# Optimization experiments

Measured on AMD Instinct MI355X. Metric: run time of the kernel, lower is better.

Reference implementation:

```python
import jax, jax.numpy as jnp
import numpy as np

N, IN_FEATS, H_FEATS, N_LAYERS, TOP_K, M = 8192, 512, 256, 2, 16, 65536


def setup_inputs() -> dict:
    key = jax.random.key(0)
    ks = jax.random.split(key, 16)
    s = 0.05
    return {
        "src": jax.random.randint(ks[0], (M,), 0, N, dtype=jnp.int32),
        "dst": jax.random.randint(ks[1], (M,), 0, N, dtype=jnp.int32),
        "labels": jax.random.uniform(ks[2], (M,), dtype=jnp.float32),
        "adj": jax.random.uniform(ks[3], (N, N), dtype=jnp.float32),
        "x": jax.random.normal(ks[4], (N, IN_FEATS), dtype=jnp.float32),
        # GNN1 layer weights
        "W1_0": jax.random.normal(ks[5], (IN_FEATS, H_FEATS), dtype=jnp.float32) * s,
        "W1_1": jax.random.normal(ks[6], (H_FEATS, H_FEATS), dtype=jnp.float32) * s,
        # GNN2 layer weights
        "W2_0": jax.random.normal(ks[7], (IN_FEATS, H_FEATS), dtype=jnp.float32) * s,
        "W2_1": jax.random.normal(ks[8], (H_FEATS, H_FEATS), dtype=jnp.float32) * s,
        # similarity-graph attention params
        "W": jax.random.normal(ks[9], (IN_FEATS, H_FEATS), dtype=jnp.float32) * s,
        "a1": jax.random.normal(ks[10], (H_FEATS, 1), dtype=jnp.float32) * s,
        "a2": jax.random.normal(ks[11], (H_FEATS, 1), dtype=jnp.float32) * s,
        # bilinear head: weight [1, in_feats, 2*h_feats], bias [1]
        "bil_w": jax.random.normal(ks[12], (1, IN_FEATS, 2 * H_FEATS), dtype=jnp.float32) * s,
        "bil_b": jnp.zeros((1,), dtype=jnp.float32),
    }


def _adj_norm(a):
    n = a.shape[0]
    a = a + jnp.eye(n, dtype=a.dtype)
    deg = a.sum(axis=0)[:, None]  # column sums, shape [n,1] (matches torch sum(dim=0).unsqueeze(1))
    return a / deg


def _gcn(a, x, weights):
    an = _adj_norm(a)
    z = x
    for Wl in weights:  # dropout=0.0 -> identity
        z = jax.nn.elu(an @ (z @ Wl))
    return z


def _sim_graph(x, W, a1, a2, top_k):
    n = x.shape[0]
    h = x @ W                      # [n, h]
    s1 = h @ a1                    # [n, 1]
    s2 = (h @ a2).reshape(1, n)    # [1, n]
    a = s1 + s2 - jnp.eye(n, dtype=x.dtype) * 1e15
    a = jax.nn.softmax(jax.nn.leaky_relu(a, 0.2), axis=1)
    kth = jax.lax.top_k(a, top_k)[0][:, -1:]  # k-th largest per row
    m = a >= kth
    m = m | m.T
    return m.astype(x.dtype)


def reference(src, dst, labels, adj, x, W1_0, W1_1, W2_0, W2_1, W, a1, a2, bil_w, bil_b):
    h = _gcn(adj, x, [W1_0, W1_1])
    sim_adj = _sim_graph(x, W, a1, a2, TOP_K)
    h_ = _gcn(sim_adj, x, [W2_0, W2_1])
    h_cat = jnp.concatenate([h, h_], axis=1)          # [n, 2h]
    src_h = x[src]                                    # [m, in_feats]
    dst_h = h_cat[dst]                                # [m, 2h]
    logits = jnp.einsum('mi,ij,mj->m', src_h, bil_w[0], dst_h) + bil_b[0]
    # BCEWithLogitsLoss (mean), numerically stable
    loss = jnp.mean(jnp.maximum(logits, 0.0) - logits * labels + jnp.log1p(jnp.exp(-jnp.abs(logits))))
    predict = logits >= 0
    return (loss, logits, predict)
```

## Files before the change

### kernel.cpp

```cpp
#include <hip/hip_runtime.h>
#include <math.h>

#define NN    8192
#define FIN   512
#define HF    256
#define ME    65536

typedef _Float16 f16x8 __attribute__((ext_vector_type(8)));
typedef __fp16 pk16x2 __attribute__((ext_vector_type(2)));
typedef float f32x4  __attribute__((ext_vector_type(4)));

__device__ inline void split_pk(float a0, float a1, unsigned& hi, unsigned& lo) {
    pk16x2 h = __builtin_amdgcn_cvt_pkrtz(a0, a1);
    float r0 = a0 - (float)h[0];
    float r1 = a1 - (float)h[1];
    pk16x2 l = __builtin_amdgcn_cvt_pkrtz(r0, r1);
    hi = __builtin_bit_cast(unsigned, h);
    lo = __builtin_bit_cast(unsigned, l);
}
__device__ inline unsigned pack_f16rn(float a0, float a1) {
    _Float16 h0 = (_Float16)a0, h1 = (_Float16)a1;
    unsigned u0 = (unsigned)__builtin_bit_cast(unsigned short, h0);
    unsigned u1 = (unsigned)__builtin_bit_cast(unsigned short, h1);
    return u0 | (u1 << 16);
}
__device__ inline void split_f16(float v, short& hi, short& lo) {
    _Float16 h = (_Float16)v;
    _Float16 l = (_Float16)(v - (float)h);
    hi = __builtin_bit_cast(short, h);
    lo = __builtin_bit_cast(short, l);
}
__device__ inline float eluf(float v) { return v > 0.f ? v : expm1f(v); }

__device__ inline void gload16(const void* g, void* l) {
    __builtin_amdgcn_global_load_lds(
        (const __attribute__((address_space(1))) unsigned int*)g,
        (__attribute__((address_space(3))) unsigned int*)l, 16, 0, 0);
}

__global__ __launch_bounds__(256) void colsum_deg(const float* __restrict__ adj,
                                                  float* __restrict__ deg) {
    int c = blockIdx.x * 256 + threadIdx.x;
    int r0 = blockIdx.y * 256;
    float s = 0.f;
    for (int r = r0; r < r0 + 256; ++r) s += adj[(size_t)r * NN + c];
    if (blockIdx.y == 0) s += 1.f;
    atomicAdd(&deg[c], s);
}

__global__ __launch_bounds__(256) void trans_w_split(const float* __restrict__ src,
                                                     short* __restrict__ dsth,
                                                     short* __restrict__ dstl,
                                                     int K, int lgN) {
    int idx = blockIdx.x * 256 + threadIdx.x;
    int N = 1 << lgN;
    int k = idx >> lgN, n = idx & (N - 1);
    short h, l;
    split_f16(src[idx], h, l);
    dsth[(size_t)n * K + k] = h;
    dstl[(size_t)n * K + k] = l;
}

__global__ __launch_bounds__(256, 2) void mfma_split(
    const float* __restrict__ A, const short* __restrict__ BtH,
    const short* __restrict__ BtL, float* __restrict__ C,
    short* __restrict__ CtH, short* __restrict__ CtL, int M, int K, int N)
{
    __shared__ __align__(16) char smem[40960];
    char* sA  = smem;
    char* sBh = smem + 8192;
    char* sBl = smem + 24576;
    float* sT = (float*)smem;
    const int tid = threadIdx.x, lane = tid & 63, wid = tid >> 6;
    const int wm = wid >> 1, wn = wid & 1;
    const int m0 = blockIdx.x * 64, n0 = blockIdx.y * 128;
    const int lhi = lane >> 4, llo = lane & 15;

    f32x4 acc[2][4];
    #pragma unroll
    for (int mi = 0; mi < 2; ++mi)
        #pragma unroll
        for (int ni = 0; ni < 4; ++ni) acc[mi][ni] = (f32x4){0.f, 0.f, 0.f, 0.f};

    for (int kt = 0; kt < K; kt += 64) {
        float4 av[4];
        #pragma unroll
        for (int it = 0; it < 4; ++it) {
            int h = tid + 256 * it;
            int r = h >> 4, hs = h & 15, slot = hs >> 1, half = hs & 1;
            int gk = ((slot ^ (r & 7)) * 2 + half) * 4;
            av[it] = *(const float4*)(A + (size_t)(m0 + r) * K + kt + gk);
        }
        __syncthreads();
        #pragma unroll
        for (int it = 0; it < 4; ++it) {
            int u = tid + 256 * it;
            int c = u >> 3, s = u & 7;
            size_t off = (size_t)(n0 + c) * K + kt + (s ^ (c & 7)) * 8;
            gload16(BtH + off, sBh + u * 16);
            gload16(BtL + off, sBl + u * 16);
        }
        #pragma unroll
        for (int it = 0; it < 4; ++it) {
            int h = tid + 256 * it;
            uint2 wh;
            wh.x = pack_f16rn(av[it].x, av[it].y);
            wh.y = pack_f16rn(av[it].z, av[it].w);
            *(uint2*)(sA + h * 8) = wh;
        }
        __syncthreads();
        #pragma unroll
        for (int ks = 0; ks < 2; ++ks) {
            f16x8 af[2], bfh[4], bfl[4];
            #pragma unroll
            for (int mi = 0; mi < 2; ++mi) {
                int R = wm * 32 + mi * 16 + llo;
                int boff = R * 128 + (((ks * 4 + lhi) ^ (R & 7)) << 4);
                af[mi] = *(const f16x8*)(sA + boff);
            }
            #pragma unroll
            for (int ni = 0; ni < 4; ++ni) {
                int Cc = wn * 64 + ni * 16 + llo;
                int boff = Cc * 128 + (((ks * 4 + lhi) ^ (Cc & 7)) << 4);
                bfh[ni] = *(const f16x8*)(sBh + boff);
                bfl[ni] = *(const f16x8*)(sBl + boff);
            }
            #pragma unroll
            for (int mi = 0; mi < 2; ++mi)
                #pragma unroll
                for (int ni = 0; ni < 4; ++ni) {
                    acc[mi][ni] = __builtin_amdgcn_mfma_f32_16x16x32_f16(af[mi], bfh[ni], acc[mi][ni], 0, 0, 0);
                    acc[mi][ni] = __builtin_amdgcn_mfma_f32_16x16x32_f16(af[mi], bfl[ni], acc[mi][ni], 0, 0, 0);
                }
        }
    }

    __syncthreads();
    #pragma unroll
    for (int mi = 0; mi < 2; ++mi)
        #pragma unroll
        for (int ni = 0; ni < 4; ++ni) {
            int lr = wm * 32 + mi * 16 + lhi * 4;
            int lc = wn * 64 + ni * 16 + llo;
            int R0 = m0 + lr;
            int Cc = n0 + lc;
            #pragma unroll
            for (int r = 0; r < 4; ++r) {
                C[(size_t)(R0 + r) * N + Cc] = acc[mi][ni][r];
                sT[(lr + r) * 136 + lc] = acc[mi][ni][r];
            }
        }
    __syncthreads();
    int c = tid >> 1, ih = (tid & 1) * 32;
    unsigned bh[16], bl[16];
    #pragma unroll
    for (int j = 0; j < 32; j += 2)
        split_pk(sT[(ih + j) * 136 + c], sT[(ih + j + 1) * 136 + c],
                 bh[j >> 1], bl[j >> 1]);
    int4* dh = (int4*)(CtH + (size_t)(n0 + c) * M + m0 + ih);
    int4* dl = (int4*)(CtL + (size_t)(n0 + c) * M + m0 + ih);
    #pragma unroll
    for (int q = 0; q < 4; ++q) { dh[q] = ((int4*)bh)[q]; dl[q] = ((int4*)bl)[q]; }
}

__global__ __launch_bounds__(256, 4) void adj_prop(const float* __restrict__ adj,
                                                   const short* __restrict__ YtH,
                                                   const short* __restrict__ YtL,
                                                   float* part0, float* part1)
{
    __shared__ __align__(16) char smem[24576];
    const int tid = threadIdx.x, lane = tid & 63, wid = tid >> 6;
    const int wm = wid >> 1, wn = wid & 1;
    const int bid = blockIdx.x;
    const int g  = bid & 7;
    const int ky = g >> 2;
    const int gx = g & 3;
    const int s  = bid >> 3;
    const int bm = gx * 32 + (s >> 2), bn = s & 3;
    const int i0 = bm * 64, c0 = bn * 64;
    const int kbase = ky * (NN / 2);
    const int lhi = lane >> 4, llo = lane & 15;

    f32x4 acc[2][2];
    #pragma unroll
    for (int mi = 0; mi < 2; ++mi)
        #pragma unroll
        for (int ni = 0; ni < 2; ++ni) acc[mi][ni] = (f32x4){0.f, 0.f, 0.f, 0.f};

    float4 avA[4], avB[4];

#define LOAD_ADJ(KT, AV)                                                        \
    {                                                                           \
        _Pragma("unroll")                                                       \
        for (int it = 0; it < 4; ++it) {                                        \
            int h = tid + 256 * it;                                             \
            int r = h >> 4, hs = h & 15, slot = hs >> 1, half = hs & 1;         \
            int gk = ((slot ^ (r & 7)) * 2 + half) * 4;                         \
            AV[it] = *(const float4*)(adj + (size_t)(i0 + r) * NN + (KT) + gk); \
        }                                                                       \
    }

#define GLOAD_B(KT)                                                             \
    {                                                                           \
        char* bh = smem + 8192;                                                 \
        char* bl = smem + 16384;                                                \
        _Pragma("unroll")                                                       \
        for (int it = 0; it < 2; ++it) {                                        \
            int u = tid + 256 * it;                                             \
            int c = u >> 3, s2 = u & 7;                                         \
            size_t off = (size_t)(c0 + c) * NN + (KT) + (s2 ^ (c & 7)) * 8;     \
            gload16(YtH + off, bh + u * 16);                                    \
            gload16(YtL + off, bl + u * 16);                                    \
        }                                                                       \
    }

#define CONVERT_A(AV)                                                           \
    {                                                                           \
        char* ah = smem;                                                        \
        _Pragma("unroll")                                                       \
        for (int it = 0; it < 4; ++it) {                                        \
            int h = tid + 256 * it;                                             \
            uint2 wh;                                                           \
            wh.x = pack_f16rn(AV[it].x, AV[it].y);                              \
            wh.y = pack_f16rn(AV[it].z, AV[it].w);                              \
            *(uint2*)(ah + h * 8) = wh;                                         \
        }                                                                       \
    }

#define DO_MFMA()                                                               \
    {                                                                           \
        const char* ah = smem;                                                  \
        const char* bh = smem + 8192;                                           \
        const char* bl = smem + 16384;                                          \
        _Pragma("unroll")                                                       \
        for (int ks = 0; ks < 2; ++ks) {                                        \
            f16x8 af[2], bfh[2], bfl[2];                                        \
            _Pragma("unroll")                                                   \
            for (int mi = 0; mi < 2; ++mi) {                                    \
                int R = wm * 32 + mi * 16 + llo;                                \
                int boff = R * 128 + (((ks * 4 + lhi) ^ (R & 7)) << 4);         \
                af[mi] = *(const f16x8*)(ah + boff);                            \
            }                                                                   \
            _Pragma("unroll")                                                   \
            for (int ni = 0; ni < 2; ++ni) {                                    \
                int Cc = wn * 32 + ni * 16 + llo;                               \
                int boff = Cc * 128 + (((ks * 4 + lhi) ^ (Cc & 7)) << 4);       \
                bfh[ni] = *(const f16x8*)(bh + boff);                           \
                bfl[ni] = *(const f16x8*)(bl + boff);                           \
            }                                                                   \
            _Pragma("unroll")                                                   \
            for (int mi = 0; mi < 2; ++mi)                                      \
                _Pragma("unroll")                                               \
                for (int ni = 0; ni < 2; ++ni) {                                \
                    acc[mi][ni] = __builtin_amdgcn_mfma_f32_16x16x32_f16(af[mi], bfh[ni], acc[mi][ni], 0, 0, 0); \
                    acc[mi][ni] = __builtin_amdgcn_mfma_f32_16x16x32_f16(af[mi], bfl[ni], acc[mi][ni], 0, 0, 0); \
                }                                                               \
        }                                                                       \
    }

    LOAD_ADJ(kbase, avA);
    LOAD_ADJ(kbase + 64, avB);
    for (int t = 0; t < 64; t += 2) {
        __syncthreads();
        GLOAD_B(kbase + t * 64);
        CONVERT_A(avA);
        __syncthreads();
        if (t + 2 < 64) LOAD_ADJ(kbase + (t + 2) * 64, avA);
        DO_MFMA();
        __syncthreads();
        GLOAD_B(kbase + (t + 1) * 64);
        CONVERT_A(avB);
        __syncthreads();
        if (t + 3 < 64) LOAD_ADJ(kbase + (t + 3) * 64, avB);
        DO_MFMA();
    }
#undef LOAD_ADJ
#undef GLOAD_B
#undef CONVERT_A
#undef DO_MFMA

    __syncthreads();
    float* sT = (float*)smem;
    #pragma unroll
    for (int mi = 0; mi < 2; ++mi)
        #pragma unroll
        for (int ni = 0; ni < 2; ++ni) {
            int lr = wm * 32 + mi * 16 + lhi * 4;
            int lc = wn * 32 + ni * 16 + llo;
            #pragma unroll
            for (int r = 0; r < 4; ++r)
                sT[(lr + r) * 68 + lc] = acc[mi][ni][r];
        }
    __syncthreads();
    float* po = ky == 0 ? part0 : part1;
    int row = tid >> 2, quad = tid & 3;
    float4* prow = (float4*)(po + (size_t)(i0 + row) * HF + c0 + quad * 16);
    #pragma unroll
    for (int q = 0; q < 4; ++q)
        prow[q] = *(const float4*)&sT[row * 68 + quad * 16 + q * 4];
}

__global__ __launch_bounds__(256) void adj_reduce(const float* part0,
                                                  const float* part1,
                                                  const float* __restrict__ Y,
                                                  const float* __restrict__ deg,
                                                  float* H) {
    int idx = blockIdx.x * 256 + threadIdx.x;
    int i = idx >> 6;
    float4 p0 = ((const float4*)part0)[idx];
    float4 p1 = ((const float4*)part1)[idx];
    float4 y  = ((const float4*)Y)[idx];
    float dinv = 1.f / deg[i];
    float4 v;
    v.x = eluf((p0.x + p1.x + y.x) * dinv);
    v.y = eluf((p0.y + p1.y + y.y) * dinv);
    v.z = eluf((p0.z + p1.z + y.z) * dinv);
    v.w = eluf((p0.w + p1.w + y.w) * dinv);
    ((float4*)H)[idx] = v;
}

__global__ __launch_bounds__(256) void gemm32(
    const float* __restrict__ A, const float* __restrict__ B,
    float* __restrict__ C, int M, int K, int N)
{
    __shared__ __align__(16) float sA[32][68];
    __shared__ __align__(16) float sB[32][68];
    const int tid = threadIdx.x;
    const int r0 = blockIdx.x * 64, c0 = blockIdx.y * 64;
    const int tr = tid >> 4, tc = tid & 15;
    float acc[4][4];
    #pragma unroll
    for (int i = 0; i < 4; ++i)
        #pragma unroll
        for (int j = 0; j < 4; ++j) acc[i][j] = 0.f;

    for (int k0 = 0; k0 < K; k0 += 32) {
        float4 av[2], bv[2];
        #pragma unroll
        for (int it = 0; it < 2; ++it) {
            int u = tid + it * 256;
            int rr = u >> 3, kk = (u & 7) * 4;
            av[it] = *(const float4*)(A + (size_t)(r0 + rr) * K + k0 + kk);
        }
        #pragma unroll
        for (int it = 0; it < 2; ++it) {
            int u = tid + it * 256;
            int br = u >> 4, bc = (u & 15) * 4;
            bv[it] = *(const float4*)(B + (size_t)(k0 + br) * N + c0 + bc);
        }
        __syncthreads();
        #pragma unroll
        for (int it = 0; it < 2; ++it) {
            int u = tid + it * 256;
            int rr = u >> 3, kk = (u & 7) * 4;
            sA[kk + 0][rr] = av[it].x; sA[kk + 1][rr] = av[it].y;
            sA[kk + 2][rr] = av[it].z; sA[kk + 3][rr] = av[it].w;
        }
        #pragma unroll
        for (int it = 0; it < 2; ++it) {
            int u = tid + it * 256;
            int br = u >> 4, bc = (u & 15) * 4;
            *(float4*)&sB[br][bc] = bv[it];
        }
        __syncthreads();
        #pragma unroll
        for (int kk = 0; kk < 32; ++kk) {
            float4 a = *(const float4*)&sA[kk][4 * tr];
            float4 b = *(const float4*)&sB[kk][4 * tc];
            float aa[4] = {a.x, a.y, a.z, a.w};
            float bb[4] = {b.x, b.y, b.z, b.w};
            #pragma unroll
            for (int i = 0; i < 4; ++i)
                #pragma unroll
                for (int j = 0; j < 4; ++j)
                    acc[i][j] = fmaf(aa[i], bb[j], acc[i][j]);
        }
        __syncthreads();
    }
    #pragma unroll
    for (int i = 0; i < 4; ++i) {
        size_t off = (size_t)(r0 + 4 * tr + i) * N + c0 + 4 * tc;
        *(float4*)(C + off) = make_float4(acc[i][0], acc[i][1], acc[i][2], acc[i][3]);
    }
}

__global__ __launch_bounds__(512) void wa2_kernel(const float* __restrict__ W,
                                                  const float* __restrict__ a2,
                                                  float* __restrict__ wa2) {
    int i = threadIdx.x;
    float s = 0.f;
    for (int j = 0; j < HF; ++j) s += W[(size_t)i * HF + j] * a2[j];
    wa2[i] = s;
}

__global__ __launch_bounds__(256) void s2_kernel(const float* __restrict__ x,
                                                 const float* __restrict__ wa2,
                                                 float* __restrict__ s2) {
    int lane = threadIdx.x & 63, wv = threadIdx.x >> 6;
    int row = blockIdx.x * 4 + wv;
    const float4* xr = (const float4*)(x + (size_t)row * FIN);
    const float4* w4 = (const float4*)wa2;
    float s = 0.f;
    #pragma unroll
    for (int t = 0; t < 2; ++t) {
        float4 a = xr[lane + 64 * t], b = w4[lane + 64 * t];
        s += a.x * b.x + a.y * b.y + a.z * b.z + a.w * b.w;
    }
    #pragma unroll
    for (int off = 32; off > 0; off >>= 1) s += __shfl_down(s, off);
    if (lane == 0) s2[row] = s;
}

__global__ __launch_bounds__(256) void top16_kernel(const float* __restrict__ s2,
                                                    int* __restrict__ Tflag) {
    __shared__ float sv[NN];
    __shared__ float rv[256];
    __shared__ int   ri[256];
    int tid = threadIdx.x;
    for (int i = tid; i < NN; i += 256) sv[i] = s2[i];
    __syncthreads();
    for (int it = 0; it < 16; ++it) {
        float best = -INFINITY; int bi = NN;
        for (int i = tid; i < NN; i += 256) {
            float v = sv[i];
            if (v > best) { best = v; bi = i; }
        }
        rv[tid] = best; ri[tid] = bi;
        __syncthreads();
        for (int off = 128; off > 0; off >>= 1) {
            if (tid < off) {
                float v2 = rv[tid + off]; int i2 = ri[tid + off];
                if (v2 > rv[tid] || (v2 == rv[tid] && i2 < ri[tid])) {
                    rv[tid] = v2; ri[tid] = i2;
                }
            }
            __syncthreads();
        }
        if (tid == 0) { int wi = ri[0]; Tflag[wi] = 1; sv[wi] = -INFINITY; }
        __syncthreads();
    }
}

__global__ __launch_bounds__(256) void colsum_T(const float* __restrict__ Y,
                                                const int* __restrict__ Tflag,
                                                float* __restrict__ total,
                                                float* __restrict__ sumT) {
    int k = threadIdx.x;
    int r0 = blockIdx.x * 128;
    float t = 0.f, tt = 0.f;
    for (int r = r0; r < r0 + 128; ++r) {
        float v = Y[(size_t)r * HF + k];
        t += v;
        if (Tflag[r]) tt += v;
    }
    atomicAdd(&total[k], t);
    atomicAdd(&sumT[k], tt);
}

__global__ __launch_bounds__(256) void gcn2_combine(float* __restrict__ Y,
                                                    const int* __restrict__ Tflag,
                                                    const float* __restrict__ sumT,
                                                    const float* __restrict__ total) {
    int idx = blockIdx.x * 256 + threadIdx.x;
    int i = idx >> 8, k = idx & 255;
    float v;
    if (Tflag[i]) v = total[k] / 8192.0f;
    else          v = (sumT[k] + Y[idx]) / 17.0f;
    Y[idx] = v > 0.f ? v : expm1f(v);
}

__global__ __launch_bounds__(256) void bilinear_kernel(
    const float* __restrict__ XB, const float* __restrict__ H,
    const float* __restrict__ Hs, const int* __restrict__ src,
    const int* __restrict__ dst, const float* __restrict__ labels,
    const float* __restrict__ bil_b,
    float* __restrict__ out_logits, float* __restrict__ out_pred,
    float* __restrict__ partials)
{
    __shared__ float wterm[4];
    int lane = threadIdx.x & 63;
    int wv = threadIdx.x >> 6;
    int e = blockIdx.x * 4 + wv;
    int s = src[e], d = dst[e];
    const float4* xb = (const float4*)(XB + (size_t)s * 512);
    const float4* h1 = (const float4*)(H + (size_t)d * HF);
    const float4* h2 = (const float4*)(Hs + (size_t)d * HF);
    float4 a = xb[lane], b = h1[lane];
    float sum = a.x * b.x + a.y * b.y + a.z * b.z + a.w * b.w;
    a = xb[64 + lane]; b = h2[lane];
    sum += a.x * b.x + a.y * b.y + a.z * b.z + a.w * b.w;
    #pragma unroll
    for (int off = 32; off > 0; off >>= 1) sum += __shfl_down(sum, off);
    if (lane == 0) {
        float l = sum + bil_b[0];
        out_logits[e] = l;
        out_pred[e] = (l >= 0.f) ? 1.f : 0.f;
        float lab = labels[e];
        wterm[wv] = fmaxf(l, 0.f) - l * lab + log1pf(expf(-fabsf(l)));
    }
    __syncthreads();
    if (threadIdx.x == 0)
        partials[blockIdx.x] = wterm[0] + wterm[1] + wterm[2] + wterm[3];
}

__global__ __launch_bounds__(256) void loss_finalize(const float* __restrict__ partials,
                                                     float* __restrict__ out) {
    __shared__ float s[256];
    int tid = threadIdx.x;
    float t = 0.f;
    for (int i = tid; i < ME / 4; i += 256) t += partials[i];
    s[tid] = t; __syncthreads();
    for (int off = 128; off > 0; off >>= 1) {
        if (tid < off) s[tid] += s[tid + off];
        __syncthreads();
    }
    if (tid == 0) out[0] = s[0] * (1.0f / (float)ME);
}

extern "C" void kernel_launch(void* const* d_in, const int* in_sizes, int n_in,
                              void* d_out, int out_size, void* d_ws, size_t ws_size,
                              hipStream_t stream) {
    const int*   src    = (const int*)d_in[0];
    const int*   dst    = (const int*)d_in[1];
    const float* labels = (const float*)d_in[2];
    const float* adj    = (const float*)d_in[3];
    const float* x      = (const float*)d_in[4];
    const float* W1_0   = (const float*)d_in[5];
    const float* W1_1   = (const float*)d_in[6];
    const float* W2_0   = (const float*)d_in[7];
    const float* W2_1   = (const float*)d_in[8];
    const float* W      = (const float*)d_in[9];
    const float* a2     = (const float*)d_in[11];
    const float* bilw   = (const float*)d_in[12];
    const float* bilb   = (const float*)d_in[13];

    float* w = (float*)d_ws;
    float* deg    = w + 0;
    float* s2v    = w + 8192;
    float* wa2v   = w + 16384;
    float* sumT   = w + 16896;
    float* total  = w + 17152;
    float* sum2T  = w + 17408;
    float* tot2   = w + 17664;
    float* lossp  = w + 17920;
    int*   Tflag  = (int*)(w + 34304);
    short* W10tH  = (short*)(w + 42496);
    short* W10tL  = (short*)(w + 108032);
    short* W11tH  = (short*)(w + 173568);
    short* W11tL  = (short*)(w + 206336);
    float* bufY   = w + 239104;
    short* YbtH   = (short*)(w + 2336256);
    short* YbtL   = (short*)(w + 3384832);
    float* bufH1  = w + 4433408;
    float* bufH   = w + 6530560;
    float* bufHs  = w + 8627712;
    float* XB     = bufY;

    float* out       = (float*)d_out;
    float* out_logit = out + 1;
    float* out_pred  = out + 1 + ME;

    hipMemsetAsync(deg, 0, NN * sizeof(float), stream);
    hipMemsetAsync(sumT, 0, 1024 * sizeof(float), stream);
    hipMemsetAsync(Tflag, 0, NN * sizeof(int), stream);

    trans_w_split<<<512, 256, 0, stream>>>(W1_0, W10tH, W10tL, 512, 8);
    trans_w_split<<<256, 256, 0, stream>>>(W1_1, W11tH, W11tL, 256, 8);

    colsum_deg<<<dim3(32, 32), 256, 0, stream>>>(adj, deg);

    mfma_split<<<dim3(128, 2), 256, 0, stream>>>(x, W10tH, W10tL, bufY, YbtH, YbtL, NN, FIN, HF);
    adj_prop<<<1024, 256, 0, stream>>>(adj, YbtH, YbtL, bufH, bufHs);
    adj_reduce<<<2048, 256, 0, stream>>>(bufH, bufHs, bufY, deg, bufH1);
    mfma_split<<<dim3(128, 2), 256, 0, stream>>>(bufH1, W11tH, W11tL, bufY, YbtH, YbtL, NN, HF, HF);
    adj_prop<<<1024, 256, 0, stream>>>(adj, YbtH, YbtL, bufH, bufHs);
    adj_reduce<<<2048, 256, 0, stream>>>(bufH, bufHs, bufY, deg, bufH);

    wa2_kernel<<<1, 512, 0, stream>>>(W, a2, wa2v);
    s2_kernel<<<NN / 4, 256, 0, stream>>>(x, wa2v, s2v);
    top16_kernel<<<1, 256, 0, stream>>>(s2v, Tflag);

    gemm32<<<dim3(128, 4), 256, 0, stream>>>(x, W2_0, bufY, NN, 512, 256);
    colsum_T<<<64, 256, 0, stream>>>(bufY, Tflag, total, sumT);
    gcn2_combine<<<NN, 256, 0, stream>>>(bufY, Tflag, sumT, total);
    gemm32<<<dim3(128, 4), 256, 0, stream>>>(bufY, W2_1, bufHs, NN, 256, 256);
    colsum_T<<<64, 256, 0, stream>>>(bufHs, Tflag, tot2, sum2T);
    gcn2_combine<<<NN, 256, 0, stream>>>(bufHs, Tflag, sum2T, tot2);

    gemm32<<<dim3(128, 8), 256, 0, stream>>>(x, bilw, XB, NN, 512, 512);
    bilinear_kernel<<<ME / 4, 256, 0, stream>>>(XB, bufH, bufHs, src, dst, labels, bilb,
                                                out_logit, out_pred, lossp);
    loss_finalize<<<1, 256, 0, stream>>>(lossp, out);
}
```

Measured before the change: 638.1 us.

## Pre-convert adjacency to fp16 during column-sum pass and stream it via LDS loads

The column-degree kernel is vectorised to float4 and, when the workspace is large enough, also writes an fp16 copy of the 8192x8192 adjacency. A new propagation kernel then streams that fp16 copy directly into shared memory with global_load_lds instead of loading fp32 and converting in registers. This halves adjacency bytes read in each of the two propagation passes, at the cost of one extra 128MB write. The new path is gated on workspace size, and the old kernel remains as a fallback. The new kernel has no software prefetch/double buffering, so each k-tile's loads are waited on before compute.

```diff
diff --git a/kernel.cpp b/kernel.cpp
--- a/kernel.cpp
+++ b/kernel.cpp
@@ -24,6 +24,9 @@
     unsigned u1 = (unsigned)__builtin_bit_cast(unsigned short, h1);
     return u0 | (u1 << 16);
 }
+__device__ inline unsigned short f16rn(float v) {
+    return __builtin_bit_cast(unsigned short, (_Float16)v);
+}
 __device__ inline void split_f16(float v, short& hi, short& lo) {
     _Float16 h = (_Float16)v;
     _Float16 l = (_Float16)(v - (float)h);
@@ -38,14 +41,26 @@
         (__attribute__((address_space(3))) unsigned int*)l, 16, 0, 0);
 }
 
-__global__ __launch_bounds__(256) void colsum_deg(const float* __restrict__ adj,
-                                                  float* __restrict__ deg) {
-    int c = blockIdx.x * 256 + threadIdx.x;
+__global__ __launch_bounds__(256) void colsum_cv(const float* __restrict__ adj,
+                                                 float* __restrict__ deg,
+                                                 unsigned short* __restrict__ adjh) {
+    int c = (blockIdx.x * 256 + threadIdx.x) * 4;
     int r0 = blockIdx.y * 256;
-    float s = 0.f;
-    for (int r = r0; r < r0 + 256; ++r) s += adj[(size_t)r * NN + c];
-    if (blockIdx.y == 0) s += 1.f;
-    atomicAdd(&deg[c], s);
+    float4 s = make_float4(0.f, 0.f, 0.f, 0.f);
+    for (int r = r0; r < r0 + 256; ++r) {
+        float4 v = *(const float4*)(adj + (size_t)r * NN + c);
+        s.x += v.x; s.y += v.y; s.z += v.z; s.w += v.w;
+        if (adjh) {
+            ushort4 h;
+            h.x = f16rn(v.x); h.y = f16rn(v.y); h.z = f16rn(v.z); h.w = f16rn(v.w);
+            *(ushort4*)(adjh + (size_t)r * NN + c) = h;
+        }
+    }
+    if (blockIdx.y == 0) { s.x += 1.f; s.y += 1.f; s.z += 1.f; s.w += 1.f; }
+    atomicAdd(&deg[c + 0], s.x);
+    atomicAdd(&deg[c + 1], s.y);
+    atomicAdd(&deg[c + 2], s.z);
+    atomicAdd(&deg[c + 3], s.w);
 }
 
 __global__ __launch_bounds__(256) void trans_w_split(const float* __restrict__ src,
@@ -163,10 +178,10 @@
     for (int q = 0; q < 4; ++q) { dh[q] = ((int4*)bh)[q]; dl[q] = ((int4*)bl)[q]; }
 }
 
-__global__ __launch_bounds__(256, 4) void adj_prop(const float* __restrict__ adj,
-                                                   const short* __restrict__ YtH,
-                                                   const short* __restrict__ YtL,
-                                                   float* part0, float* part1)
+__global__ __launch_bounds__(256, 4) void adj_prop_g(const unsigned short* __restrict__ adjh,
+                                                     const short* __restrict__ YtH,
+                                                     const short* __restrict__ YtL,
+                                                     float* part0, float* part1)
 {
     __shared__ __align__(16) char smem[24576];
     const int tid = threadIdx.x, lane = tid & 63, wid = tid >> 6;
@@ -187,6 +202,101 @@
         #pragma unroll
         for (int ni = 0; ni < 2; ++ni) acc[mi][ni] = (f32x4){0.f, 0.f, 0.f, 0.f};
 
+    for (int t = 0; t < 64; ++t) {
+        const int KT = kbase + t * 64;
+        __syncthreads();
+        #pragma unroll
+        for (int it = 0; it < 2; ++it) {
+            int u = tid + 256 * it;
+            int r = u >> 3, sq = u & 7;
+            gload16(adjh + (size_t)(i0 + r) * NN + KT + ((sq ^ (r & 7)) * 8),
+                    smem + u * 16);
+        }
+        #pragma unroll
+        for (int it = 0; it < 2; ++it) {
+            int u = tid + 256 * it;
+            int c = u >> 3, sq = u & 7;
+            size_t off = (size_t)(c0 + c) * NN + KT + (sq ^ (c & 7)) * 8;
+            gload16(YtH + off, smem + 8192 + u * 16);
+            gload16(YtL + off, smem + 16384 + u * 16);
+        }
+        __syncthreads();
+        {
+            const char* ah = smem;
+            const char* bh = smem + 8192;
+            const char* bl = smem + 16384;
+            #pragma unroll
+            for (int ks = 0; ks < 2; ++ks) {
+                f16x8 af[2], bfh[2], bfl[2];
+                #pragma unroll
+                for (int mi = 0; mi < 2; ++mi) {
+                    int R = wm * 32 + mi * 16 + llo;
+                    int boff = R * 128 + (((ks * 4 + lhi) ^ (R & 7)) << 4);
+                    af[mi] = *(const f16x8*)(ah + boff);
+                }
+                #pragma unroll
+                for (int ni = 0; ni < 2; ++ni) {
+                    int Cc = wn * 32 + ni * 16 + llo;
+                    int boff = Cc * 128 + (((ks * 4 + lhi) ^ (Cc & 7)) << 4);
+                    bfh[ni] = *(const f16x8*)(bh + boff);
+                    bfl[ni] = *(const f16x8*)(bl + boff);
+                }
+                #pragma unroll
+                for (int mi = 0; mi < 2; ++mi)
+                    #pragma unroll
+                    for (int ni = 0; ni < 2; ++ni) {
+                        acc[mi][ni] = __builtin_amdgcn_mfma_f32_16x16x32_f16(af[mi], bfh[ni], acc[mi][ni], 0, 0, 0);
+                        acc[mi][ni] = __builtin_amdgcn_mfma_f32_16x16x32_f16(af[mi], bfl[ni], acc[mi][ni], 0, 0, 0);
+                    }
+            }
+        }
+    }
+
+    __syncthreads();
+    float* sT = (float*)smem;
+    #pragma unroll
+    for (int mi = 0; mi < 2; ++mi)
+        #pragma unroll
+        for (int ni = 0; ni < 2; ++ni) {
+            int lr = wm * 32 + mi * 16 + lhi * 4;
+            int lc = wn * 32 + ni * 16 + llo;
+            #pragma unroll
+            for (int r = 0; r < 4; ++r)
+                sT[(lr + r) * 68 + lc] = acc[mi][ni][r];
+        }
+    __syncthreads();
+    float* po = ky == 0 ? part0 : part1;
+    int row = tid >> 2, quad = tid & 3;
+    float4* prow = (float4*)(po + (size_t)(i0 + row) * HF + c0 + quad * 16);
+    #pragma unroll
+    for (int q = 0; q < 4; ++q)
+        prow[q] = *(const float4*)&sT[row * 68 + quad * 16 + q * 4];
+}
+
+__global__ __launch_bounds__(256, 4) void adj_prop_cv(const float* __restrict__ adj,
+                                                      const short* __restrict__ YtH,
+                                                      const short* __restrict__ YtL,
+                                                      float* part0, float* part1)
+{
+    __shared__ __align__(16) char smem[24576];
+    const int tid = threadIdx.x, lane = tid & 63, wid = tid >> 6;
+    const int wm = wid >> 1, wn = wid & 1;
+    const int bid = blockIdx.x;
+    const int g  = bid & 7;
+    const int ky = g >> 2;
+    const int gx = g & 3;
+    const int s  = bid >> 3;
+    const int bm = gx * 32 + (s >> 2), bn = s & 3;
+    const int i0 = bm * 64, c0 = bn * 64;
+    const int kbase = ky * (NN / 2);
+    const int lhi = lane >> 4, llo = lane & 15;
+
+    f32x4 acc[2][2];
+    #pragma unroll
+    for (int mi = 0; mi < 2; ++mi)
+        #pragma unroll
+        for (int ni = 0; ni < 2; ++ni) acc[mi][ni] = (f32x4){0.f, 0.f, 0.f, 0.f};
+
     float4 avA[4], avB[4];
 
 #define LOAD_ADJ(KT, AV)                                                        \
@@ -199,34 +309,28 @@
             AV[it] = *(const float4*)(adj + (size_t)(i0 + r) * NN + (KT) + gk); \
         }                                                                       \
     }
-
 #define GLOAD_B(KT)                                                             \
     {                                                                           \
-        char* bh = smem + 8192;                                                 \
-        char* bl = smem + 16384;                                                \
         _Pragma("unroll")                                                       \
         for (int it = 0; it < 2; ++it) {                                        \
             int u = tid + 256 * it;                                             \
             int c = u >> 3, s2 = u & 7;                                         \
             size_t off = (size_t)(c0 + c) * NN + (KT) + (s2 ^ (c & 7)) * 8;     \
-            gload16(YtH + off, bh + u * 16);                                    \
-            gload16(YtL + off, bl + u * 16);                                    \
+            gload16(YtH + off, smem + 8192 + u * 16);                           \
+            gload16(YtL + off, smem + 16384 + u * 16);                          \
         }                                                                       \
     }
-
 #define CONVERT_A(AV)                                                           \
     {                                                                           \
-        char* ah = smem;                                                        \
         _Pragma("unroll")                                                       \
         for (int it = 0; it < 4; ++it) {                                        \
             int h = tid + 256 * it;                                             \
             uint2 wh;                                                           \
             wh.x = pack_f16rn(AV[it].x, AV[it].y);                              \
             wh.y = pack_f16rn(AV[it].z, AV[it].w);                              \
-            *(uint2*)(ah + h * 8) = wh;                                         \
+            *(uint2*)(smem + h * 8) = wh;                                       \
         }                                                                       \
     }
-
 #define DO_MFMA()                                                               \
     {                                                                           \
         const char* ah = smem;                                                  \
@@ -554,7 +658,9 @@
     float* bufH1  = w + 4433408;
     float* bufH   = w + 6530560;
     float* bufHs  = w + 8627712;
+    unsigned short* adjh = (unsigned short*)(w + 10724864);
     float* XB     = bufY;
+    const bool big = ws_size >= (size_t)44279296 * sizeof(float);
 
     float* out       = (float*)d_out;
     float* out_logit = out + 1;
@@ -567,13 +673,15 @@
     trans_w_split<<<512, 256, 0, stream>>>(W1_0, W10tH, W10tL, 512, 8);
     trans_w_split<<<256, 256, 0, stream>>>(W1_1, W11tH, W11tL, 256, 8);
 
-    colsum_deg<<<dim3(32, 32), 256, 0, stream>>>(adj, deg);
+    colsum_cv<<<dim3(8, 32), 256, 0, stream>>>(adj, deg, big ? adjh : nullptr);
 
     mfma_split<<<dim3(128, 2), 256, 0, stream>>>(x, W10tH, W10tL, bufY, YbtH, YbtL, NN, FIN, HF);
-    adj_prop<<<1024, 256, 0, stream>>>(adj, YbtH, YbtL, bufH, bufHs);
+    if (big) adj_prop_g<<<1024, 256, 0, stream>>>(adjh, YbtH, YbtL, bufH, bufHs);
+    else     adj_prop_cv<<<1024, 256, 0, stream>>>(adj, YbtH, YbtL, bufH, bufHs);
     adj_reduce<<<2048, 256, 0, stream>>>(bufH, bufHs, bufY, deg, bufH1);
     mfma_split<<<dim3(128, 2), 256, 0, stream>>>(bufH1, W11tH, W11tL, bufY, YbtH, YbtL, NN, HF, HF);
-    adj_prop<<<1024, 256, 0, stream>>>(adj, YbtH, YbtL, bufH, bufHs);
+    if (big) adj_prop_g<<<1024, 256, 0, stream>>>(adjh, YbtH, YbtL, bufH, bufHs);
+    else     adj_prop_cv<<<1024, 256, 0, stream>>>(adj, YbtH, YbtL, bufH, bufHs);
     adj_reduce<<<2048, 256, 0, stream>>>(bufH, bufHs, bufY, deg, bufH);
 
     wa2_kernel<<<1, 512, 0, stream>>>(W, a2, wa2v);
```

Result: slower. 702.9 us (+10.2%).
